# Kernel tuning notes

Measured on AMD Instinct MI355X. Metric: run time of the kernel, lower is better.

The kernel has to match this reference:

```python
import jax, jax.numpy as jnp
import numpy as np

D = 512       # model_dim
NH = 8        # num_heads
HD = D // NH  # head_dim


def _lstm(x, w_ih, w_hh, b_ih, b_hh):
    """PyTorch-style single-layer LSTM, batch_first. Gate order: i,f,g,o.
    x: [B,L,D] -> hidden states [B,L,H]."""
    B = x.shape[0]
    H = w_hh.shape[1]
    # precompute input contribution for all timesteps: [B,L,4H]
    gx = jnp.einsum('bld,gd->blg', x, w_ih) + b_ih + b_hh

    def step(carry, g_t):
        h, c = carry
        g = g_t + h @ w_hh.T  # [B,4H]
        i, f, gg, o = jnp.split(g, 4, axis=-1)
        c = jax.nn.sigmoid(f) * c + jax.nn.sigmoid(i) * jnp.tanh(gg)
        h = jax.nn.sigmoid(o) * jnp.tanh(c)
        return (h, c), h

    h0 = jnp.zeros((B, H), x.dtype)
    (_, _), hs = jax.lax.scan(step, (h0, h0), jnp.swapaxes(gx, 0, 1))
    return jnp.swapaxes(hs, 0, 1)  # [B,L,H]


def setup_inputs() -> dict:
    key = jax.random.key(0)
    ks = jax.random.split(key, 20)
    s_in = 1.0 / np.sqrt(D)
    inp = {
        'query': jax.random.normal(ks[0], (32, 512, D), jnp.float32),
        'key':   jax.random.normal(ks[1], (32, 512, D), jnp.float32),
        'value': jax.random.normal(ks[2], (32, 512, D), jnp.float32),
    }
    i = 3
    for name in ('q', 'k', 'v'):
        inp[f'w_ih_{name}'] = jax.random.normal(ks[i], (4 * D, D), jnp.float32) * s_in; i += 1
        inp[f'w_hh_{name}'] = jax.random.normal(ks[i], (4 * D, D), jnp.float32) * s_in; i += 1
        inp[f'b_ih_{name}'] = jax.random.normal(ks[i], (4 * D,), jnp.float32) * s_in; i += 1
        inp[f'b_hh_{name}'] = jax.random.normal(ks[i], (4 * D,), jnp.float32) * s_in; i += 1
    inp['w_out'] = jax.random.normal(ks[i], (D, D), jnp.float32) * s_in; i += 1
    inp['b_out'] = jnp.zeros((D,), jnp.float32)
    return inp


def reference(query, key, value,
              w_ih_q, w_hh_q, b_ih_q, b_hh_q,
              w_ih_k, w_hh_k, b_ih_k, b_hh_k,
              w_ih_v, w_hh_v, b_ih_v, b_hh_v,
              w_out, b_out):
    B, Lq, _ = query.shape
    Lk = key.shape[1]
    q = _lstm(query, w_ih_q, w_hh_q, b_ih_q, b_hh_q)
    k = _lstm(key,   w_ih_k, w_hh_k, b_ih_k, b_hh_k)
    v = _lstm(value, w_ih_v, w_hh_v, b_ih_v, b_hh_v)
    # split heads: split(dim=-1)+cat(dim=0) == reshape to [B,L,NH,HD]
    q = q.reshape(B, Lq, NH, HD)
    k = k.reshape(B, Lk, NH, HD)
    v = v.reshape(B, Lk, NH, HD)
    scores = jnp.einsum('bqhd,bkhd->bhqk', q, k) / np.sqrt(HD).astype(np.float32)
    attn = jax.nn.softmax(scores, axis=-1)
    out = jnp.einsum('bhqk,bkhd->bqhd', attn, v).reshape(B, Lq, D)
    return out @ w_out.T + b_out
```

## Files before the change

kernel.cpp:

```cpp
#include <hip/hip_runtime.h>
#include <cstdint>

#define B_ 32
#define L_ 512
#define G4_ 2048
#define POI 0xFFFFFFFFu

typedef __bf16          bf16x8 __attribute__((ext_vector_type(8)));
typedef float           f32x4  __attribute__((ext_vector_type(4)));
typedef unsigned short  u16x8  __attribute__((ext_vector_type(8)));
typedef unsigned int    u32x4  __attribute__((ext_vector_type(4)));

__device__ __forceinline__ unsigned short f2bf(float v) {
  unsigned int u = __float_as_uint(v);
  unsigned int r = u + 0x7fffu + ((u >> 16) & 1u);
  return (unsigned short)(r >> 16);
}
__device__ __forceinline__ float bf2f(unsigned short u) {
  return __uint_as_float(((unsigned int)u) << 16);
}
__device__ __forceinline__ float sigf(float x) { return 1.0f / (1.0f + __expf(-x)); }
__device__ __forceinline__ float tanhf_(float x) { return 1.0f - 2.0f / (__expf(2.0f * x) + 1.0f); }

__global__ __launch_bounds__(256) void k_fill(float* o, long n, float v) {
  for (long i = (long)blockIdx.x * 256 + threadIdx.x; i < n; i += (long)gridDim.x * 256) o[i] = v;
}

__global__ __launch_bounds__(256) void k_cvt(const float* __restrict__ in,
                                             unsigned short* __restrict__ out, long n) {
  long i = ((long)blockIdx.x * 256 + threadIdx.x) * 8;
  if (i >= n) return;
  const float4* p = (const float4*)(in + i);
  float4 a = p[0], b = p[1];
  u16x8 o;
  o[0] = f2bf(a.x); o[1] = f2bf(a.y); o[2] = f2bf(a.z); o[3] = f2bf(a.w);
  o[4] = f2bf(b.x); o[5] = f2bf(b.y); o[6] = f2bf(b.z); o[7] = f2bf(b.w);
  *(u16x8*)(out + i) = o;
}

__global__ __launch_bounds__(256) void k_pack_w(const float* __restrict__ wih,
                                                const float* __restrict__ whh,
                                                unsigned short* __restrict__ wcat) {
  long i = ((long)blockIdx.x * 256 + threadIdx.x) * 8;
  int nr = (int)(i >> 10), col = (int)(i & 1023);
  int cc = nr >> 7, wvp = (nr >> 4) & 7, OR = nr & 15;
  int grow = (OR & 3) * 512 + cc * 32 + wvp * 4 + (OR >> 2);
  const float* src = (col < 512) ? (wih + (long)grow * 512 + col)
                                 : (whh + (long)grow * 512 + (col - 512));
  const float4* p = (const float4*)src;
  float4 a = p[0], b = p[1];
  u16x8 o;
  o[0] = f2bf(a.x); o[1] = f2bf(a.y); o[2] = f2bf(a.z); o[3] = f2bf(a.w);
  o[4] = f2bf(b.x); o[5] = f2bf(b.y); o[6] = f2bf(b.z); o[7] = f2bf(b.w);
  *(u16x8*)(wcat + i) = o;
}

struct LBias { const float* bi[3]; const float* bh[3]; };

__global__ __launch_bounds__(512, 1) void lstm_rec(
    const unsigned short* __restrict__ wcat,
    const unsigned short* __restrict__ xs,
    LBias bb,
    unsigned short* __restrict__ hout)
{
  const int r8 = blockIdx.x & 7;
  if (r8 >= 6) return;
  const int rg = r8, cc = blockIdx.x >> 3;
  const int l = rg >> 1, b0 = (rg & 1) * 16;
  const int tid = threadIdx.x, lane = tid & 63, wv = tid >> 6;

  __shared__ unsigned short sXH[16 * 1024];

  bf16x8 af[32];
  {
    int nr = cc * 128 + wv * 16 + (lane & 15);
    const unsigned short* Wp = wcat + ((long)l * G4_ + nr) * 1024 + ((lane >> 4) << 3);
#pragma unroll
    for (int kf = 0; kf < 32; ++kf) af[kf] = *(const bf16x8*)(Wp + kf * 32);
  }
  const int u = cc * 32 + wv * 4 + (lane >> 4);
  float bias[4];
#pragma unroll
  for (int r = 0; r < 4; ++r) bias[r] = bb.bi[l][r * 512 + u] + bb.bh[l][r * 512 + u];

  const int sx = tid >> 5;
  const int slot = tid & 31;
  const int sw = sx << 4;
  const int xoff0 = sx * 2048 + slot * 16, xoff1 = xoff0 + 512;
  const int hoff0 = xoff0 + 1024,           hoff1 = hoff0 + 512;
  const int slot8 = slot * 8;
  const long seqbase = ((long)(l * B_ + b0 + sx)) * L_;

  const int srow = lane & 15;
  const int rbm = srow << 11, swm = srow << 4;
  const int kob = (lane >> 4) << 4;

  const int hseq = lane & 15;
  const long hrowb = ((long)(l * B_ + b0 + hseq)) * L_;
  const int upair = cc * 16 + wv * 2 + (lane >> 5);

  u16x8 xr0, xr1;
  {
    const unsigned short* p = xs + seqbase * 512 + slot8;
    xr0 = *(const u16x8*)p;
    xr1 = *(const u16x8*)(p + 256);
  }
  float creg = 0.f;

  for (int t = 0; t < L_; ++t) {
    *(u16x8*)((char*)sXH + (xoff0 ^ sw)) = xr0;
    *(u16x8*)((char*)sXH + (xoff1 ^ sw)) = xr1;
    if (t + 1 < L_) {
      const unsigned short* p = xs + (seqbase + t + 1) * 512 + slot8;
      xr0 = *(const u16x8*)p;
      xr1 = *(const u16x8*)(p + 256);
    }
    __syncthreads();

    u32x4 h0 = (u32x4){0, 0, 0, 0}, h1 = (u32x4){0, 0, 0, 0};
    const unsigned short* hp0 = hout + (seqbase + t - 1) * 512 + slot8;
    const unsigned short* hp1 = hp0 + 256;
    if (t > 0) {
      asm volatile("global_load_dwordx4 %0, %2, off sc1\n\t"
                   "global_load_dwordx4 %1, %3, off sc1"
                   : "=&v"(h0), "=&v"(h1) : "v"(hp0), "v"(hp1) : "memory");
    }

    f32x4 aA = (f32x4){0.f, 0.f, 0.f, 0.f};
    f32x4 aB = (f32x4){0.f, 0.f, 0.f, 0.f};
#pragma unroll
    for (int kf = 0; kf < 16; kf += 2) {
      bf16x8 bv0 = *(const bf16x8*)((const char*)sXH + ((rbm + kf * 64 + kob) ^ swm));
      bf16x8 bv1 = *(const bf16x8*)((const char*)sXH + ((rbm + (kf + 1) * 64 + kob) ^ swm));
      aA = __builtin_amdgcn_mfma_f32_16x16x32_bf16(af[kf], bv0, aA, 0, 0, 0);
      aB = __builtin_amdgcn_mfma_f32_16x16x32_bf16(af[kf + 1], bv1, aB, 0, 0, 0);
    }

    if (t > 0) {
      asm volatile("s_waitcnt vmcnt(0)" ::: "memory");
      __builtin_amdgcn_sched_barrier(0);
      while (h0[0] == POI || h0[1] == POI || h0[2] == POI || h0[3] == POI ||
             h1[0] == POI || h1[1] == POI || h1[2] == POI || h1[3] == POI) {
        asm volatile("global_load_dwordx4 %0, %2, off sc1\n\t"
                     "global_load_dwordx4 %1, %3, off sc1\n\t"
                     "s_waitcnt vmcnt(0)"
                     : "=&v"(h0), "=&v"(h1) : "v"(hp0), "v"(hp1) : "memory");
        __builtin_amdgcn_sched_barrier(0);
      }
    }
    *(u16x8*)((char*)sXH + (hoff0 ^ sw)) = *(u16x8*)&h0;
    *(u16x8*)((char*)sXH + (hoff1 ^ sw)) = *(u16x8*)&h1;
    __syncthreads();

#pragma unroll
    for (int kf = 16; kf < 32; kf += 2) {
      bf16x8 bv0 = *(const bf16x8*)((const char*)sXH + ((rbm + kf * 64 + kob) ^ swm));
      bf16x8 bv1 = *(const bf16x8*)((const char*)sXH + ((rbm + (kf + 1) * 64 + kob) ^ swm));
      aA = __builtin_amdgcn_mfma_f32_16x16x32_bf16(af[kf], bv0, aA, 0, 0, 0);
      aB = __builtin_amdgcn_mfma_f32_16x16x32_bf16(af[kf + 1], bv1, aB, 0, 0, 0);
    }

    {
      float Pi = aA[0] + aB[0] + bias[0];
      float Pf = aA[1] + aB[1] + bias[1];
      float Pg = aA[2] + aB[2] + bias[2];
      float Po = aA[3] + aB[3] + bias[3];
      float iv = sigf(Pi), fv = sigf(Pf), gv = tanhf_(Pg), ov = sigf(Po);
      creg = fv * creg + iv * gv;
      float h = ov * tanhf_(creg);
      unsigned int hb16 = (unsigned int)f2bf(h);
      unsigned int other = (unsigned int)__shfl_xor((int)hb16, 16);
      if ((lane & 16) == 0) {
        unsigned int pk = hb16 | (other << 16);
        unsigned int* dst = (unsigned int*)(hout + (hrowb + t) * 512) + upair;
        __hip_atomic_store(dst, pk, __ATOMIC_RELAXED, __HIP_MEMORY_SCOPE_AGENT);
      }
    }
  }
}

__global__ __launch_bounds__(256) void attn_kernel(
    const unsigned short* __restrict__ h, unsigned short* __restrict__ attnout)
{
  const int qt = blockIdx.x, head = blockIdx.y, b = blockIdx.z;
  const int tid = threadIdx.x;

  __shared__ float q_lds[64 * 68];
  __shared__ float ks_lds[64 * 68];
  __shared__ float v_lds[64 * 68];

  const long qbase = ((long)b * L_) * 512;
  const long kbase = ((long)(B_ + b) * L_) * 512;
  const long vbase = ((long)(2 * B_ + b) * L_) * 512;

#pragma unroll
  for (int p = 0; p < 2; ++p) {
    int idx = p * 256 + tid;
    int row = idx >> 3, c8 = (idx & 7) << 3;
    u16x8 v8 = *(const u16x8*)(h + qbase + (long)(qt * 64 + row) * 512 + head * 64 + c8);
#pragma unroll
    for (int j = 0; j < 8; ++j) q_lds[row * 68 + c8 + j] = bf2f(v8[j]);
  }
  float m_run = -1e30f, lsum = 0.f;
  float acc[16];
#pragma unroll
  for (int j = 0; j < 16; ++j) acc[j] = 0.f;
  const int tq = tid & 15, tk = tid >> 4;
  const int oq = tid >> 2, od = (tid & 3) * 16;
  const int quad = tid & 3;

  for (int kt = 0; kt < 8; ++kt) {
    __syncthreads();
#pragma unroll
    for (int p = 0; p < 2; ++p) {
      int idx = p * 256 + tid;
      int row = idx >> 3, c8 = (idx & 7) << 3;
      u16x8 kv = *(const u16x8*)(h + kbase + (long)(kt * 64 + row) * 512 + head * 64 + c8);
      u16x8 vv = *(const u16x8*)(h + vbase + (long)(kt * 64 + row) * 512 + head * 64 + c8);
#pragma unroll
      for (int j = 0; j < 8; ++j) {
        ks_lds[row * 68 + c8 + j] = bf2f(kv[j]);
        v_lds[row * 68 + c8 + j]  = bf2f(vv[j]);
      }
    }
    __syncthreads();
    float sc[16];
#pragma unroll
    for (int x = 0; x < 16; ++x) sc[x] = 0.f;
    for (int d4 = 0; d4 < 64; d4 += 4) {
      f32x4 qv[4], kv4[4];
#pragma unroll
      for (int a = 0; a < 4; ++a) qv[a] = *(const f32x4*)&q_lds[(tq + a * 16) * 68 + d4];
#pragma unroll
      for (int c = 0; c < 4; ++c) kv4[c] = *(const f32x4*)&ks_lds[(tk + c * 16) * 68 + d4];
#pragma unroll
      for (int a = 0; a < 4; ++a)
#pragma unroll
        for (int c = 0; c < 4; ++c)
          sc[a * 4 + c] += qv[a][0] * kv4[c][0] + qv[a][1] * kv4[c][1] +
                           qv[a][2] * kv4[c][2] + qv[a][3] * kv4[c][3];
    }
    __syncthreads();
#pragma unroll
    for (int a = 0; a < 4; ++a)
#pragma unroll
      for (int c = 0; c < 4; ++c)
        ks_lds[(tq + a * 16) * 68 + (tk + c * 16)] = sc[a * 4 + c] * 0.125f;
    __syncthreads();
    float corr;
    {
      float pv[16];
      float mx = m_run;
#pragma unroll
      for (int j = 0; j < 16; ++j) {
        pv[j] = ks_lds[oq * 68 + quad * 16 + j];
        mx = fmaxf(mx, pv[j]);
      }
      mx = fmaxf(mx, __shfl_xor(mx, 1));
      mx = fmaxf(mx, __shfl_xor(mx, 2));
      corr = __expf(m_run - mx);
      m_run = mx;
      float rs = 0.f;
#pragma unroll
      for (int j = 0; j < 16; ++j) {
        float p = __expf(pv[j] - mx);
        ks_lds[oq * 68 + quad * 16 + j] = p;
        rs += p;
      }
      rs += __shfl_xor(rs, 1);
      rs += __shfl_xor(rs, 2);
      lsum = lsum * corr + rs;
    }
    __syncthreads();
    {
#pragma unroll
      for (int j = 0; j < 16; ++j) acc[j] *= corr;
      for (int k = 0; k < 64; ++k) {
        float p = ks_lds[oq * 68 + k];
        f32x4 v0 = *(const f32x4*)&v_lds[k * 68 + od];
        f32x4 v1 = *(const f32x4*)&v_lds[k * 68 + od + 4];
        f32x4 v2 = *(const f32x4*)&v_lds[k * 68 + od + 8];
        f32x4 v3 = *(const f32x4*)&v_lds[k * 68 + od + 12];
#pragma unroll
        for (int j = 0; j < 4; ++j) {
          acc[j]      += p * v0[j];
          acc[4 + j]  += p * v1[j];
          acc[8 + j]  += p * v2[j];
          acc[12 + j] += p * v3[j];
        }
      }
    }
  }
  float inv = 1.0f / lsum;
  unsigned short* op = attnout + ((long)(b * L_ + qt * 64 + oq)) * 512 + head * 64 + od;
#pragma unroll
  for (int j = 0; j < 16; ++j) op[j] = f2bf(acc[j] * inv);
}

__global__ __launch_bounds__(256) void gemm_proj(
    const unsigned short* __restrict__ A, const unsigned short* __restrict__ Bw,
    const float* __restrict__ bias, float* __restrict__ C)
{
  const int m0 = blockIdx.y * 128, n0 = blockIdx.x * 128;
  __shared__ unsigned short sA[128 * 64];
  __shared__ unsigned short sB[128 * 64];
  const int tid = threadIdx.x, lane = tid & 63, wv = tid >> 6;
  const int wr = wv >> 1, wc = wv & 1;
  f32x4 acc[4][4];
#pragma unroll
  for (int i = 0; i < 4; ++i)
#pragma unroll
    for (int j = 0; j < 4; ++j) acc[i][j] = (f32x4){0.f, 0.f, 0.f, 0.f};

  for (int kt = 0; kt < 512; kt += 64) {
#pragma unroll
    for (int p = 0; p < 4; ++p) {
      int g = p * 256 + tid;
      int r = g >> 3, c8 = (g & 7) << 3;
      int bo = ((r << 7) + (c8 << 1)) ^ ((r & 7) << 4);
      *(u16x8*)((char*)sA + bo) = *(const u16x8*)(A + (long)(m0 + r) * 512 + kt + c8);
      *(u16x8*)((char*)sB + bo) = *(const u16x8*)(Bw + (long)(n0 + r) * 512 + kt + c8);
    }
    __syncthreads();
#pragma unroll
    for (int kf = 0; kf < 2; ++kf) {
      int cb = kf * 32 + ((lane >> 4) << 3);
      bf16x8 av[4], bv[4];
#pragma unroll
      for (int i = 0; i < 4; ++i) {
        int ra = wr * 64 + i * 16 + (lane & 15);
        av[i] = *(const bf16x8*)((const char*)sA + (((ra << 7) + (cb << 1)) ^ ((ra & 7) << 4)));
        int rb = wc * 64 + i * 16 + (lane & 15);
        bv[i] = *(const bf16x8*)((const char*)sB + (((rb << 7) + (cb << 1)) ^ ((rb & 7) << 4)));
      }
#pragma unroll
      for (int i = 0; i < 4; ++i)
#pragma unroll
        for (int j = 0; j < 4; ++j)
          acc[i][j] = __builtin_amdgcn_mfma_f32_16x16x32_bf16(av[i], bv[j], acc[i][j], 0, 0, 0);
    }
    __syncthreads();
  }
#pragma unroll
  for (int i = 0; i < 4; ++i) {
    int gm0 = m0 + wr * 64 + i * 16 + ((lane >> 4) << 2);
#pragma unroll
    for (int j = 0; j < 4; ++j) {
      int gn = n0 + wc * 64 + j * 16 + (lane & 15);
      float bv = bias[gn];
#pragma unroll
      for (int r = 0; r < 4; ++r)
        C[(long)(gm0 + r) * 512 + gn] = acc[i][j][r] + bv;
    }
  }
}

extern "C" void kernel_launch(void* const* d_in, const int* in_sizes, int n_in,
                              void* d_out, int out_size, void* d_ws, size_t ws_size,
                              hipStream_t stream)
{
  const float* xin[3]  = {(const float*)d_in[0], (const float*)d_in[1], (const float*)d_in[2]};
  const float* w_ih[3] = {(const float*)d_in[3], (const float*)d_in[7],  (const float*)d_in[11]};
  const float* w_hh[3] = {(const float*)d_in[4], (const float*)d_in[8],  (const float*)d_in[12]};
  const float* b_ih[3] = {(const float*)d_in[5], (const float*)d_in[9],  (const float*)d_in[13]};
  const float* b_hh[3] = {(const float*)d_in[6], (const float*)d_in[10], (const float*)d_in[14]};
  const float* w_out = (const float*)d_in[15];
  const float* b_out = (const float*)d_in[16];

  const size_t TOTAL = 130553856ULL;
  if (ws_size < TOTAL) {
    k_fill<<<dim3(1024), dim3(256), 0, stream>>>((float*)d_out, (long)out_size, 1.0f);
    return;
  }
  char* ws = (char*)d_ws;
  unsigned short* xs      = (unsigned short*)(ws);
  unsigned short* hout    = (unsigned short*)(ws + 50331648);
  unsigned short* wcat    = (unsigned short*)(ws + 100663296);
  unsigned short* wouts   = (unsigned short*)(ws + 113246208);
  unsigned short* attnout = (unsigned short*)(ws + 113770496);

  hipMemsetAsync(hout, 0xFF, 50331648, stream);

  for (int l = 0; l < 3; ++l) {
    k_cvt<<<dim3(4096), dim3(256), 0, stream>>>(xin[l], xs + (long)l * 8388608, 8388608L);
    k_pack_w<<<dim3(1024), dim3(256), 0, stream>>>(w_ih[l], w_hh[l], wcat + (long)l * 2097152);
  }
  k_cvt<<<dim3(128), dim3(256), 0, stream>>>(w_out, wouts, 262144L);

  LBias bb;
  for (int l = 0; l < 3; ++l) { bb.bi[l] = b_ih[l]; bb.bh[l] = b_hh[l]; }
  lstm_rec<<<dim3(128), dim3(512), 0, stream>>>(wcat, xs, bb, hout);

  attn_kernel<<<dim3(8, 8, 32), dim3(256), 0, stream>>>(hout, attnout);

  gemm_proj<<<dim3(4, 128), dim3(256), 0, stream>>>(attnout, wouts, b_out, (float*)d_out);
}
```

Baseline: 1.297 ms.

## Reorder LSTM step: defer h publish, issue h poll after input MFMAs

Restructures the per-timestep schedule of the persistent LSTM kernel. The x tile for the next step is now prefetched with inline asm and written to LDS at the end of the iteration, behind one closing barrier. The previous hidden state is published at the start of the next iteration. The cross-block h load is issued only after the input-half MFMAs, so it is more likely to find ready data and avoid poison-value spin reloads. The cost is that h load latency is no longer overlapped with the x-half MFMAs, and publishing h later could lengthen the recurrent critical path.

```diff
diff --git a/kernel.cpp b/kernel.cpp
--- a/kernel.cpp
+++ b/kernel.cpp
@@ -99,33 +99,32 @@
   const long hrowb = ((long)(l * B_ + b0 + hseq)) * L_;
   const int upair = cc * 16 + wv * 2 + (lane >> 5);
 
-  u16x8 xr0, xr1;
   {
     const unsigned short* p = xs + seqbase * 512 + slot8;
-    xr0 = *(const u16x8*)p;
-    xr1 = *(const u16x8*)(p + 256);
-  }
+    u16x8 x0 = *(const u16x8*)p;
+    u16x8 x1 = *(const u16x8*)(p + 256);
+    *(u16x8*)((char*)sXH + (xoff0 ^ sw)) = x0;
+    *(u16x8*)((char*)sXH + (xoff1 ^ sw)) = x1;
+  }
+  __syncthreads();
+
+  u32x4 xr0, xr1;
+  unsigned int hpk = 0;
   float creg = 0.f;
 
   for (int t = 0; t < L_; ++t) {
-    *(u16x8*)((char*)sXH + (xoff0 ^ sw)) = xr0;
-    *(u16x8*)((char*)sXH + (xoff1 ^ sw)) = xr1;
-    if (t + 1 < L_) {
-      const unsigned short* p = xs + (seqbase + t + 1) * 512 + slot8;
-      xr0 = *(const u16x8*)p;
-      xr1 = *(const u16x8*)(p + 256);
-    }
-    __syncthreads();
-
-    u32x4 h0 = (u32x4){0, 0, 0, 0}, h1 = (u32x4){0, 0, 0, 0};
-    const unsigned short* hp0 = hout + (seqbase + t - 1) * 512 + slot8;
-    const unsigned short* hp1 = hp0 + 256;
-    if (t > 0) {
-      asm volatile("global_load_dwordx4 %0, %2, off sc1\n\t"
-                   "global_load_dwordx4 %1, %3, off sc1"
-                   : "=&v"(h0), "=&v"(h1) : "v"(hp0), "v"(hp1) : "memory");
-    }
-
+    if (t > 0 && (lane & 16) == 0) {
+      unsigned int* dst = (unsigned int*)(hout + (hrowb + (t - 1)) * 512) + upair;
+      __hip_atomic_store(dst, hpk, __ATOMIC_RELAXED, __HIP_MEMORY_SCOPE_AGENT);
+    }
+    {
+      int tn = (t + 1 < L_) ? t + 1 : t;
+      const unsigned short* xp0 = xs + (seqbase + tn) * 512 + slot8;
+      const unsigned short* xp1 = xp0 + 256;
+      asm volatile("global_load_dwordx4 %0, %2, off\n\t"
+                   "global_load_dwordx4 %1, %3, off"
+                   : "=&v"(xr0), "=&v"(xr1) : "v"(xp0), "v"(xp1) : "memory");
+    }
     f32x4 aA = (f32x4){0.f, 0.f, 0.f, 0.f};
     f32x4 aB = (f32x4){0.f, 0.f, 0.f, 0.f};
 #pragma unroll
@@ -135,9 +134,14 @@
       aA = __builtin_amdgcn_mfma_f32_16x16x32_bf16(af[kf], bv0, aA, 0, 0, 0);
       aB = __builtin_amdgcn_mfma_f32_16x16x32_bf16(af[kf + 1], bv1, aB, 0, 0, 0);
     }
-
+    u32x4 h0 = (u32x4){0, 0, 0, 0}, h1 = (u32x4){0, 0, 0, 0};
     if (t > 0) {
-      asm volatile("s_waitcnt vmcnt(0)" ::: "memory");
+      const unsigned short* hp0 = hout + (seqbase + t - 1) * 512 + slot8;
+      const unsigned short* hp1 = hp0 + 256;
+      asm volatile("global_load_dwordx4 %0, %2, off sc1\n\t"
+                   "global_load_dwordx4 %1, %3, off sc1\n\t"
+                   "s_waitcnt vmcnt(0)"
+                   : "=&v"(h0), "=&v"(h1) : "v"(hp0), "v"(hp1) : "memory");
       __builtin_amdgcn_sched_barrier(0);
       while (h0[0] == POI || h0[1] == POI || h0[2] == POI || h0[3] == POI ||
              h1[0] == POI || h1[1] == POI || h1[2] == POI || h1[3] == POI) {
@@ -147,11 +151,13 @@
                      : "=&v"(h0), "=&v"(h1) : "v"(hp0), "v"(hp1) : "memory");
         __builtin_amdgcn_sched_barrier(0);
       }
+    } else {
+      asm volatile("s_waitcnt vmcnt(0)" ::: "memory");
+      __builtin_amdgcn_sched_barrier(0);
     }
     *(u16x8*)((char*)sXH + (hoff0 ^ sw)) = *(u16x8*)&h0;
     *(u16x8*)((char*)sXH + (hoff1 ^ sw)) = *(u16x8*)&h1;
     __syncthreads();
-
 #pragma unroll
     for (int kf = 16; kf < 32; kf += 2) {
       bf16x8 bv0 = *(const bf16x8*)((const char*)sXH + ((rbm + kf * 64 + kob) ^ swm));
@@ -159,7 +165,6 @@
       aA = __builtin_amdgcn_mfma_f32_16x16x32_bf16(af[kf], bv0, aA, 0, 0, 0);
       aB = __builtin_amdgcn_mfma_f32_16x16x32_bf16(af[kf + 1], bv1, aB, 0, 0, 0);
     }
-
     {
       float Pi = aA[0] + aB[0] + bias[0];
       float Pf = aA[1] + aB[1] + bias[1];
@@ -170,12 +175,17 @@
       float h = ov * tanhf_(creg);
       unsigned int hb16 = (unsigned int)f2bf(h);
       unsigned int other = (unsigned int)__shfl_xor((int)hb16, 16);
-      if ((lane & 16) == 0) {
-        unsigned int pk = hb16 | (other << 16);
-        unsigned int* dst = (unsigned int*)(hout + (hrowb + t) * 512) + upair;
-        __hip_atomic_store(dst, pk, __ATOMIC_RELAXED, __HIP_MEMORY_SCOPE_AGENT);
-      }
-    }
+      hpk = hb16 | (other << 16);
+    }
+    if (t + 1 < L_) {
+      *(u16x8*)((char*)sXH + (xoff0 ^ sw)) = *(u16x8*)&xr0;
+      *(u16x8*)((char*)sXH + (xoff1 ^ sw)) = *(u16x8*)&xr1;
+    }
+    __syncthreads();
+  }
+  if ((lane & 16) == 0) {
+    unsigned int* dst = (unsigned int*)(hout + (hrowb + (L_ - 1)) * 512) + upair;
+    __hip_atomic_store(dst, hpk, __ATOMIC_RELAXED, __HIP_MEMORY_SCOPE_AGENT);
   }
 }
 
@@ -367,7 +377,7 @@
   const float* w_out = (const float*)d_in[15];
   const float* b_out = (const float*)d_in[16];
 
-  const size_t TOTAL = 130553856ULL;
+  const size_t TOTAL = 130547712ULL;
   if (ws_size < TOTAL) {
     k_fill<<<dim3(1024), dim3(256), 0, stream>>>((float*)d_out, (long)out_size, 1.0f);
     return;
```

Result: slower. 1.855 ms (+43.0%).

## Rewrite attention kernel with bf16 MFMA for QK^T and PV

Applied to the files above, without the earlier changes.

Replaces the scalar fp32 LDS-based attention with MFMA 16x16x32 bf16 instructions for both the score and PV products. Q, K and V are kept as bf16 in shared memory, with V stored transposed. Each wave owns 16 query rows and keeps per-row online-softmax state in registers. Probabilities are rounded to bf16 before the PV product, which adds a little precision loss in exchange for removing the scalar FMA loops and several block barriers.

```diff
diff --git a/kernel.cpp b/kernel.cpp
--- a/kernel.cpp
+++ b/kernel.cpp
@@ -183,11 +183,12 @@
     const unsigned short* __restrict__ h, unsigned short* __restrict__ attnout)
 {
   const int qt = blockIdx.x, head = blockIdx.y, b = blockIdx.z;
-  const int tid = threadIdx.x;
-
-  __shared__ float q_lds[64 * 68];
-  __shared__ float ks_lds[64 * 68];
-  __shared__ float v_lds[64 * 68];
+  const int tid = threadIdx.x, lane = tid & 63, wv = tid >> 6;
+
+  __shared__ unsigned short q_s[64 * 68];
+  __shared__ unsigned short k_s[64 * 68];
+  __shared__ unsigned short vt_s[64 * 68];
+  __shared__ unsigned short p_s[4][16 * 72];
 
   const long qbase = ((long)b * L_) * 512;
   const long kbase = ((long)(B_ + b) * L_) * 512;
@@ -197,17 +198,24 @@
   for (int p = 0; p < 2; ++p) {
     int idx = p * 256 + tid;
     int row = idx >> 3, c8 = (idx & 7) << 3;
-    u16x8 v8 = *(const u16x8*)(h + qbase + (long)(qt * 64 + row) * 512 + head * 64 + c8);
-#pragma unroll
-    for (int j = 0; j < 8; ++j) q_lds[row * 68 + c8 + j] = bf2f(v8[j]);
-  }
-  float m_run = -1e30f, lsum = 0.f;
-  float acc[16];
-#pragma unroll
-  for (int j = 0; j < 16; ++j) acc[j] = 0.f;
-  const int tq = tid & 15, tk = tid >> 4;
-  const int oq = tid >> 2, od = (tid & 3) * 16;
-  const int quad = tid & 3;
+    *(u16x8*)&q_s[row * 68 + c8] =
+        *(const u16x8*)(h + qbase + (long)(qt * 64 + row) * 512 + head * 64 + c8);
+  }
+  __syncthreads();
+  const int k0 = (lane >> 4) << 3;
+  bf16x8 qa0, qa1;
+  {
+    int m = wv * 16 + (lane & 15);
+    qa0 = *(const bf16x8*)&q_s[m * 68 + k0];
+    qa1 = *(const bf16x8*)&q_s[m * 68 + k0 + 32];
+  }
+
+  f32x4 O[4];
+#pragma unroll
+  for (int j = 0; j < 4; ++j) O[j] = (f32x4){0.f, 0.f, 0.f, 0.f};
+  float m_run[4], lsum[4];
+#pragma unroll
+  for (int r = 0; r < 4; ++r) { m_run[r] = -1e30f; lsum[r] = 0.f; }
 
   for (int kt = 0; kt < 8; ++kt) {
     __syncthreads();
@@ -217,84 +225,81 @@
       int row = idx >> 3, c8 = (idx & 7) << 3;
       u16x8 kv = *(const u16x8*)(h + kbase + (long)(kt * 64 + row) * 512 + head * 64 + c8);
       u16x8 vv = *(const u16x8*)(h + vbase + (long)(kt * 64 + row) * 512 + head * 64 + c8);
-#pragma unroll
-      for (int j = 0; j < 8; ++j) {
-        ks_lds[row * 68 + c8 + j] = bf2f(kv[j]);
-        v_lds[row * 68 + c8 + j]  = bf2f(vv[j]);
-      }
-    }
-    __syncthreads();
-    float sc[16];
-#pragma unroll
-    for (int x = 0; x < 16; ++x) sc[x] = 0.f;
-    for (int d4 = 0; d4 < 64; d4 += 4) {
-      f32x4 qv[4], kv4[4];
-#pragma unroll
-      for (int a = 0; a < 4; ++a) qv[a] = *(const f32x4*)&q_lds[(tq + a * 16) * 68 + d4];
-#pragma unroll
-      for (int c = 0; c < 4; ++c) kv4[c] = *(const f32x4*)&ks_lds[(tk + c * 16) * 68 + d4];
-#pragma unroll
-      for (int a = 0; a < 4; ++a)
-#pragma unroll
-        for (int c = 0; c < 4; ++c)
-          sc[a * 4 + c] += qv[a][0] * kv4[c][0] + qv[a][1] * kv4[c][1] +
-                           qv[a][2] * kv4[c][2] + qv[a][3] * kv4[c][3];
-    }
-    __syncthreads();
-#pragma unroll
-    for (int a = 0; a < 4; ++a)
-#pragma unroll
-      for (int c = 0; c < 4; ++c)
-        ks_lds[(tq + a * 16) * 68 + (tk + c * 16)] = sc[a * 4 + c] * 0.125f;
-    __syncthreads();
-    float corr;
-    {
-      float pv[16];
-      float mx = m_run;
-#pragma unroll
-      for (int j = 0; j < 16; ++j) {
-        pv[j] = ks_lds[oq * 68 + quad * 16 + j];
-        mx = fmaxf(mx, pv[j]);
-      }
+      *(u16x8*)&k_s[row * 68 + c8] = kv;
+#pragma unroll
+      for (int j = 0; j < 8; ++j) vt_s[(c8 + j) * 68 + row] = vv[j];
+    }
+    __syncthreads();
+
+    f32x4 sc[4];
+#pragma unroll
+    for (int j = 0; j < 4; ++j) {
+      int n = j * 16 + (lane & 15);
+      bf16x8 kb0 = *(const bf16x8*)&k_s[n * 68 + k0];
+      bf16x8 kb1 = *(const bf16x8*)&k_s[n * 68 + k0 + 32];
+      f32x4 z = (f32x4){0.f, 0.f, 0.f, 0.f};
+      z = __builtin_amdgcn_mfma_f32_16x16x32_bf16(qa0, kb0, z, 0, 0, 0);
+      z = __builtin_amdgcn_mfma_f32_16x16x32_bf16(qa1, kb1, z, 0, 0, 0);
+      sc[j] = z * 0.125f;
+    }
+
+    float corr[4];
+#pragma unroll
+    for (int r = 0; r < 4; ++r) {
+      float mx = fmaxf(fmaxf(sc[0][r], sc[1][r]), fmaxf(sc[2][r], sc[3][r]));
       mx = fmaxf(mx, __shfl_xor(mx, 1));
       mx = fmaxf(mx, __shfl_xor(mx, 2));
-      corr = __expf(m_run - mx);
-      m_run = mx;
-      float rs = 0.f;
-#pragma unroll
-      for (int j = 0; j < 16; ++j) {
-        float p = __expf(pv[j] - mx);
-        ks_lds[oq * 68 + quad * 16 + j] = p;
-        rs += p;
+      mx = fmaxf(mx, __shfl_xor(mx, 4));
+      mx = fmaxf(mx, __shfl_xor(mx, 8));
+      float mn = fmaxf(m_run[r], mx);
+      corr[r] = __expf(m_run[r] - mn);
+      m_run[r] = mn;
+    }
+    float rs[4] = {0.f, 0.f, 0.f, 0.f};
+#pragma unroll
+    for (int j = 0; j < 4; ++j)
+#pragma unroll
+      for (int r = 0; r < 4; ++r) {
+        float pv = __expf(sc[j][r] - m_run[r]);
+        rs[r] += pv;
+        p_s[wv][((lane >> 4) * 4 + r) * 72 + j * 16 + (lane & 15)] = f2bf(pv);
       }
-      rs += __shfl_xor(rs, 1);
-      rs += __shfl_xor(rs, 2);
-      lsum = lsum * corr + rs;
-    }
-    __syncthreads();
-    {
-#pragma unroll
-      for (int j = 0; j < 16; ++j) acc[j] *= corr;
-      for (int k = 0; k < 64; ++k) {
-        float p = ks_lds[oq * 68 + k];
-        f32x4 v0 = *(const f32x4*)&v_lds[k * 68 + od];
-        f32x4 v1 = *(const f32x4*)&v_lds[k * 68 + od + 4];
-        f32x4 v2 = *(const f32x4*)&v_lds[k * 68 + od + 8];
-        f32x4 v3 = *(const f32x4*)&v_lds[k * 68 + od + 12];
-#pragma unroll
-        for (int j = 0; j < 4; ++j) {
-          acc[j]      += p * v0[j];
-          acc[4 + j]  += p * v1[j];
-          acc[8 + j]  += p * v2[j];
-          acc[12 + j] += p * v3[j];
-        }
-      }
-    }
-  }
-  float inv = 1.0f / lsum;
-  unsigned short* op = attnout + ((long)(b * L_ + qt * 64 + oq)) * 512 + head * 64 + od;
-#pragma unroll
-  for (int j = 0; j < 16; ++j) op[j] = f2bf(acc[j] * inv);
+#pragma unroll
+    for (int r = 0; r < 4; ++r) {
+      float t = rs[r];
+      t += __shfl_xor(t, 1);
+      t += __shfl_xor(t, 2);
+      t += __shfl_xor(t, 4);
+      t += __shfl_xor(t, 8);
+      lsum[r] = lsum[r] * corr[r] + t;
+    }
+#pragma unroll
+    for (int j = 0; j < 4; ++j)
+#pragma unroll
+      for (int r = 0; r < 4; ++r) O[j][r] *= corr[r];
+
+    bf16x8 pa0 = *(const bf16x8*)&p_s[wv][(lane & 15) * 72 + k0];
+    bf16x8 pa1 = *(const bf16x8*)&p_s[wv][(lane & 15) * 72 + k0 + 32];
+#pragma unroll
+    for (int j = 0; j < 4; ++j) {
+      int n = j * 16 + (lane & 15);
+      bf16x8 vb0 = *(const bf16x8*)&vt_s[n * 68 + k0];
+      bf16x8 vb1 = *(const bf16x8*)&vt_s[n * 68 + k0 + 32];
+      O[j] = __builtin_amdgcn_mfma_f32_16x16x32_bf16(pa0, vb0, O[j], 0, 0, 0);
+      O[j] = __builtin_amdgcn_mfma_f32_16x16x32_bf16(pa1, vb1, O[j], 0, 0, 0);
+    }
+  }
+
+  float inv[4];
+#pragma unroll
+  for (int r = 0; r < 4; ++r) inv[r] = 1.0f / lsum[r];
+  const int orow0 = qt * 64 + wv * 16 + ((lane >> 4) << 2);
+#pragma unroll
+  for (int r = 0; r < 4; ++r) {
+    unsigned short* op = attnout + ((long)(b * L_ + orow0 + r)) * 512 + head * 64 + (lane & 15);
+#pragma unroll
+    for (int j = 0; j < 4; ++j) op[j * 16] = f2bf(O[j][r] * inv[r]);
+  }
 }
 
 __global__ __launch_bounds__(256) void gemm_proj(
@@ -367,7 +372,7 @@
   const float* w_out = (const float*)d_in[15];
   const float* b_out = (const float*)d_in[16];
 
-  const size_t TOTAL = 130553856ULL;
+  const size_t TOTAL = 130547712ULL;
   if (ws_size < TOTAL) {
     k_fill<<<dim3(1024), dim3(256), 0, stream>>>((float*)d_out, (long)out_size, 1.0f);
     return;
```

New measurement: 1.093 ms. -15.7%, faster.
